# Kernel optimization log

Measured on AMD Instinct MI355X. Metric: run time of the kernel, lower is better.

The kernel has to match this reference:

```python
import math
import jax, jax.numpy as jnp
import numpy as np

B, C_IN, H, W = 16, 384, 64, 64
CDIM, K, NSCALES, ITERS = 128, 64, 2, 3

def conv1x1(x, w, b):
    # x: [B,C,H,W], w: [O,C], b: [O]
    return jnp.einsum('bchw,oc->bohw', x, w) + b[None, :, None, None]

def mlp2(x, w1, b1, w2, b2):
    return conv1x1(jax.nn.relu(conv1x1(x, w1, b1)), w2, b2)

def log_optimal_transport(scores, dustbin, iters):
    B_, K_, N_ = scores.shape
    Z = jnp.concatenate([scores, dustbin], axis=1)  # [B,K+1,N]
    log_mu = jnp.full((B_, K_ + 1), -math.log(K_ + 1), dtype=scores.dtype)
    log_nu = jnp.full((B_, N_), -math.log(N_), dtype=scores.dtype)
    u = jnp.zeros_like(log_mu)
    v = jnp.zeros_like(log_nu)
    for _ in range(iters):
        u = log_mu - jax.nn.logsumexp(Z + v[:, None, :], axis=2)
        v = log_nu - jax.nn.logsumexp(Z + u[:, :, None], axis=1)
    return Z + u[:, :, None] + v[:, None, :]

def avg_pool2(x):
    b, c, h, w = x.shape
    return x.reshape(b, c, h // 2, 2, w // 2, 2).mean(axis=(3, 5))

def scale_branch(xs, fw1, fb1, fw2, fb2, sw1, sb1, sw2, sb2, dw1, db1, dw2, db2):
    b = xs.shape[0]
    local_feat = mlp2(xs, fw1, fb1, fw2, fb2).reshape(b, CDIM, -1)   # [B,C,N]
    score = mlp2(xs, sw1, sb1, sw2, sb2).reshape(b, K, -1)           # [B,K,N]
    dustbin = mlp2(xs, dw1, db1, dw2, db2).reshape(b, 1, -1)         # [B,1,N]
    log_p = log_optimal_transport(score, dustbin, ITERS)
    p = jnp.exp(log_p)[:, :-1, :]                                    # drop dustbin row
    p = p / (p.sum(axis=-1, keepdims=True) + 1e-8)
    out = jnp.einsum('bcn,bkn->bck', local_feat, p)                  # [B,C,K]
    out = out / jnp.clip(jnp.linalg.norm(out, axis=1, keepdims=True), 1e-12)
    return out.reshape(b, -1), local_feat

def setup_inputs():
    key = jax.random.key(0)
    ks = jax.random.split(key, 13)
    inp = {'x': jax.random.normal(ks[0], (B, C_IN, H, W), jnp.float32)}
    kidx = 1
    for s in range(NSCALES):
        for name, (o, i) in [('fw1', (512, C_IN)), ('fw2', (CDIM, 512)),
                              ('sw1', (512, C_IN)), ('sw2', (K, 512)),
                              ('dw1', (128, C_IN)), ('dw2', (1, 128))]:
            inp[f'{name}_{s}'] = 0.02 * jax.random.normal(ks[kidx % 13], (o, i), jnp.float32)
            inp[f'{name[0]}b{name[2]}_{s}'] = jnp.zeros((o,), jnp.float32)
            kidx += 1
    return inp

def reference(x,
              fw1_0, fb1_0, fw2_0, fb2_0, sw1_0, sb1_0, sw2_0, sb2_0, dw1_0, db1_0, dw2_0, db2_0,
              fw1_1, fb1_1, fw2_1, fb2_1, sw1_1, sb1_1, sw2_1, sb2_1, dw1_1, db1_1, dw2_1, db2_1):
    params = [
        (fw1_0, fb1_0, fw2_0, fb2_0, sw1_0, sb1_0, sw2_0, sb2_0, dw1_0, db1_0, dw2_0, db2_0),
        (fw1_1, fb1_1, fw2_1, fb2_1, sw1_1, sb1_1, sw2_1, sb2_1, dw1_1, db1_1, dw2_1, db2_1),
    ]
    descs = []
    xs = x
    for s in range(NSCALES):
        if s > 0:
            xs = avg_pool2(xs)
        d, _ = scale_branch(xs, *params[s])
        descs.append(d)
    g = jnp.stack(descs, axis=1).mean(axis=1)
    g = g / jnp.clip(jnp.linalg.norm(g, axis=1, keepdims=True), 1e-12)
    return g
```

## Files before the change

### kernel.cpp

```cpp
#include <hip/hip_runtime.h>
#include <math.h>

typedef __attribute__((ext_vector_type(8))) short short8;
typedef __attribute__((ext_vector_type(4))) float floatx4;

__device__ inline float bf2f(short s) {
    union { unsigned u; float f; } x; x.u = ((unsigned)(unsigned short)s) << 16; return x.f;
}
__device__ inline short f2bf(float f) {
    union { float f; unsigned u; } x; x.f = f;
    unsigned r = x.u + 0x7fff + ((x.u >> 16) & 1);
    return (short)(r >> 16);
}

struct WSet {
    const float *fw1, *fb1, *fw2, *sw1, *sb1, *sw2, *sb2, *dw1, *db1, *dw2, *db2;
};

__global__ __launch_bounds__(256) void wprep(WSet a0, WSet a1,
    short* __restrict__ W1f, short* __restrict__ W2af, short* __restrict__ W2bf,
    float* __restrict__ B1p, float* __restrict__ B2bp)
{
    const int s = blockIdx.y;
    const WSet A = s ? a1 : a0;
    W1f  += (size_t)s * 491520;
    W2af += (size_t)s * 65536;
    W2bf += (size_t)s * 98304;
    B1p  += s * 1280;
    B2bp += s * 128;
    int id = blockIdx.x * 256 + threadIdx.x;
    if (id < 491520) {
        int e = id & 7, l = (id >> 3) & 63, g = (id >> 9) & 15, rest = id >> 13;
        int kc = rest % 12, c = rest / 12;
        int m = c * 256 + g * 16 + (l & 15);
        int k = kc * 32 + (l >> 4) * 8 + e;
        float v = 0.f;
        if (m < 512) v = A.fw1[m * 384 + k];
        else if (m < 1024) v = A.sw1[(m - 512) * 384 + k];
        else if (m < 1152) v = A.dw1[(m - 1024) * 384 + k];
        W1f[id] = f2bf(v);
        return;
    }
    id -= 491520;
    if (id < 65536) {
        int e = id & 7, l = (id >> 3) & 63, g = (id >> 9) & 7, ka = id >> 12;
        int r = g * 16 + (l & 15), k = ka * 32 + (l >> 4) * 8 + e;
        W2af[id] = f2bf(A.fw2[r * 512 + k]);
        return;
    }
    id -= 65536;
    if (id < 98304) {
        int e = id & 7, l = (id >> 3) & 63, g = (id >> 9) & 7, kb = id >> 12;
        int r = g * 16 + (l & 15), krel = kb * 32 + (l >> 4) * 8 + e;
        float v = 0.f;
        if (r < 64 && krel < 512) v = A.sw2[r * 512 + krel];
        else if (r == 64 && krel >= 512 && krel < 640) v = A.dw2[krel - 512];
        W2bf[id] = f2bf(v);
        return;
    }
    id -= 98304;
    if (id < 1280) {
        float v = 0.f;
        if (id < 512) v = A.fb1[id];
        else if (id < 1024) v = A.sb1[id - 512];
        else if (id < 1152) v = A.db1[id - 1024];
        B1p[id] = v;
        return;
    }
    id -= 1280;
    if (id < 128) B2bp[id] = id < 64 ? A.sb2[id] : id == 64 ? A.db2[0] : 0.f;
}

__global__ __launch_bounds__(256) void xprep(const float* __restrict__ x,
                                             short* __restrict__ xT, short* __restrict__ x1T)
{
    __shared__ float xt[64 * 129];
    const int ip = blockIdx.x;
    const int cg = blockIdx.y;
    const int b  = blockIdx.z;
    const int t  = threadIdx.x;
    #pragma unroll
    for (int u = 0; u < 8; u++) {
        int idx = t + 256 * u;
        int c = idx >> 5, spq = idx & 31;
        float4 v = *(const float4*)&x[(((long)b * 384 + cg * 64 + c) * 64 + ip * 2 + (spq >> 4)) * 64 + (spq & 15) * 4];
        float* d = &xt[c * 129 + spq * 4];
        d[0] = v.x; d[1] = v.y; d[2] = v.z; d[3] = v.w;
    }
    __syncthreads();
    {
        int sp = t >> 1, ch = t & 1;
        short tmp[32];
        #pragma unroll
        for (int cc = 0; cc < 32; cc++) tmp[cc] = f2bf(xt[(ch * 32 + cc) * 129 + sp]);
        short* dst = xT + ((long)b * 4096 + ip * 128 + sp) * 384 + cg * 64 + ch * 32;
        #pragma unroll
        for (int v = 0; v < 4; v++) *(short8*)(dst + v * 8) = *(short8*)(tmp + v * 8);
    }
    {
        int j1 = t >> 3, c8 = t & 7;
        short tmp[8];
        #pragma unroll
        for (int e = 0; e < 8; e++) {
            int c = c8 * 8 + e;
            float v = 0.25f * (xt[c * 129 + j1 * 2]      + xt[c * 129 + j1 * 2 + 1] +
                               xt[c * 129 + 64 + j1 * 2] + xt[c * 129 + 64 + j1 * 2 + 1]);
            tmp[e] = f2bf(v);
        }
        *(short8*)(x1T + ((long)b * 1024 + ip * 32 + j1) * 384 + cg * 64 + c8 * 8) = *(short8*)tmp;
    }
}

__global__ __launch_bounds__(512, 4) void fused_mlp(
    const short* __restrict__ W1f_, const float* __restrict__ B1p_,
    const short* __restrict__ W2af_, const float* __restrict__ fb2_0, const float* __restrict__ fb2_1,
    const short* __restrict__ W2bf_, const float* __restrict__ B2bp_,
    const short* __restrict__ xT, const short* __restrict__ x1T,
    float* __restrict__ feat0, float* __restrict__ feat1,
    short* __restrict__ Eg0, short* __restrict__ Eg1,
    float* __restrict__ pu0, float* __restrict__ pu1)
{
    __shared__ short xs[12 * 2048];
    __shared__ short hs[8 * 2048];
    const int tid = threadIdx.x;
    const int wid = tid >> 6, lane = tid & 63;
    const int l15 = lane & 15, q = lane >> 4;
    const int bx = blockIdx.x, b = blockIdx.y;
    const int sc = bx >= 64;
    const int tile = sc ? bx - 64 : bx;
    const int N = sc ? 1024 : 4096;
    const int n0 = tile * 64;
    const short* XT = sc ? x1T : xT;
    const short* W1f = W1f_ + (size_t)sc * 491520;
    const float* B1p = B1p_ + sc * 1280;
    const short* W2af = W2af_ + (size_t)sc * 65536;
    const short* W2bf = W2bf_ + (size_t)sc * 98304;
    const float* fb2 = sc ? fb2_1 : fb2_0;
    const float* B2bp = B2bp_ + sc * 128;
    float* feat = (sc ? feat1 : feat0) + (long)b * 128 * N;
    short* Eg = (sc ? Eg1 : Eg0) + (long)b * 65 * N;
    float* pu = sc ? pu1 : pu0;
    const int npart = sc ? 16 : 64;

    {
        const int n = tid >> 3;
        const int c0 = (tid & 7) * 6;
        const short* src = XT + ((long)b * N + n0 + n) * 384 + c0 * 8;
        const int jj = n >> 4, nl = n & 15;
        #pragma unroll
        for (int i = 0; i < 6; i++) {
            int c = c0 + i;
            int kc = c >> 2, qq = c & 3;
            *(short8*)(xs + kc * 2048 + jj * 512 + ((qq << 4) | nl) * 8) =
                *(const short8*)(src + i * 8);
        }
    }
    __syncthreads();

    floatx4 acc2[2][4];
    #pragma unroll
    for (int i = 0; i < 2; i++)
        #pragma unroll
        for (int j = 0; j < 4; j++) acc2[i][j] = floatx4{0.f, 0.f, 0.f, 0.f};

    auto phase2 = [&](int pc) {
        if (pc < 2) {
            const short* WA = W2af + (size_t)pc * 32768;
            short8 hb[2][4], wa[2];
            #pragma unroll
            for (int j = 0; j < 4; j++) hb[0][j] = *(short8*)(hs + j * 512 + lane * 8);
            wa[0] = *(const short8*)(WA + wid * 512 + lane * 8);
            #pragma unroll
            for (int kc2 = 0; kc2 < 8; kc2++) {
                short8 bfr[4];
                #pragma unroll
                for (int j = 0; j < 4; j++) bfr[j] = hb[kc2 & 1][j];
                short8 aF = wa[kc2 & 1];
                if (kc2 + 1 < 8) {
                    #pragma unroll
                    for (int j = 0; j < 4; j++)
                        hb[(kc2 + 1) & 1][j] = *(short8*)(hs + (kc2 + 1) * 2048 + j * 512 + lane * 8);
                    wa[(kc2 + 1) & 1] = *(const short8*)(WA + ((kc2 + 1) * 8 + wid) * 512 + lane * 8);
                }
                #pragma unroll
                for (int j = 0; j < 4; j++)
                    acc2[0][j] = __builtin_amdgcn_mfma_f32_16x16x32_bf16(aF, bfr[j], acc2[0][j], 0, 0, 0);
            }
        } else {
            if (wid >= 5) return;
            const short* WB = W2bf + (size_t)(pc - 2) * 32768;
            short8 hb[2][4], we[2];
            #pragma unroll
            for (int j = 0; j < 4; j++) hb[0][j] = *(short8*)(hs + j * 512 + lane * 8);
            we[0] = *(const short8*)(WB + wid * 512 + lane * 8);
            #pragma unroll
            for (int kc2 = 0; kc2 < 8; kc2++) {
                short8 bfr[4];
                #pragma unroll
                for (int j = 0; j < 4; j++) bfr[j] = hb[kc2 & 1][j];
                short8 aE = we[kc2 & 1];
                if (kc2 + 1 < 8) {
                    #pragma unroll
                    for (int j = 0; j < 4; j++)
                        hb[(kc2 + 1) & 1][j] = *(short8*)(hs + (kc2 + 1) * 2048 + j * 512 + lane * 8);
                    we[(kc2 + 1) & 1] = *(const short8*)(WB + ((kc2 + 1) * 8 + wid) * 512 + lane * 8);
                }
                #pragma unroll
                for (int j = 0; j < 4; j++)
                    acc2[1][j] = __builtin_amdgcn_mfma_f32_16x16x32_bf16(aE, bfr[j], acc2[1][j], 0, 0, 0);
            }
        }
    };

    for (int c = 0; c < 5; c++) {
        if (c > 0) phase2(c - 1);
        floatx4 acc1[2][4];
        #pragma unroll
        for (int i = 0; i < 2; i++)
            #pragma unroll
            for (int j = 0; j < 4; j++) acc1[i][j] = floatx4{0.f, 0.f, 0.f, 0.f};
        const short* Wb = W1f + (long)c * 98304;
        short8 abuf[2][2];
        #pragma unroll
        for (int i = 0; i < 2; i++) {
            abuf[0][i] = *(const short8*)(Wb + (wid * 2 + i) * 512 + lane * 8);
            abuf[1][i] = *(const short8*)(Wb + (16 + wid * 2 + i) * 512 + lane * 8);
        }
        #pragma unroll
        for (int kc = 0; kc < 12; kc++) {
            short8 ac[2], bc[4];
            #pragma unroll
            for (int i = 0; i < 2; i++) ac[i] = abuf[kc & 1][i];
            #pragma unroll
            for (int j = 0; j < 4; j++) bc[j] = *(short8*)(xs + kc * 2048 + j * 512 + lane * 8);
            if (kc + 2 < 12) {
                #pragma unroll
                for (int i = 0; i < 2; i++)
                    abuf[kc & 1][i] = *(const short8*)(Wb + ((kc + 2) * 16 + wid * 2 + i) * 512 + lane * 8);
            }
            #pragma unroll
            for (int i = 0; i < 2; i++)
                #pragma unroll
                for (int j = 0; j < 4; j++)
                    acc1[i][j] = __builtin_amdgcn_mfma_f32_16x16x32_bf16(ac[i], bc[j], acc1[i][j], 0, 0, 0);
        }
        __syncthreads();
        #pragma unroll
        for (int i = 0; i < 2; i++) {
            const int qf = i * 2 + (q >> 1);
            const int e0 = 4 * (q & 1);
            const int mrow = c * 256 + wid * 32 + i * 16 + q * 4;
            float bw[4];
            #pragma unroll
            for (int rr = 0; rr < 4; rr++) bw[rr] = B1p[mrow + rr];
            #pragma unroll
            for (int j = 0; j < 4; j++) {
                short pk[4];
                #pragma unroll
                for (int rr = 0; rr < 4; rr++)
                    pk[rr] = f2bf(fmaxf(acc1[i][j][rr] + bw[rr], 0.f));
                *(unsigned long long*)(hs + wid * 2048 + j * 512 + ((qf << 4) | l15) * 8 + e0) =
                    *(unsigned long long*)pk;
            }
        }
        __syncthreads();
    }
    phase2(4);

    {
        const int row0 = wid * 16 + q * 4;
        #pragma unroll
        for (int rr = 0; rr < 4; rr++) {
            float bv = fb2[row0 + rr];
            #pragma unroll
            for (int j = 0; j < 4; j++)
                feat[(long)(row0 + rr) * N + n0 + 16 * j + l15] = acc2[0][j][rr] + bv;
        }
    }
    __syncthreads();
    float* puld = (float*)hs;
    if (wid < 4) {
        #pragma unroll
        for (int rr = 0; rr < 4; rr++) {
            int row = wid * 16 + q * 4 + rr;
            float bv = B2bp[row];
            float s = 0.f;
            #pragma unroll
            for (int j = 0; j < 4; j++) {
                float e = expf(acc2[1][j][rr] + bv);
                Eg[(long)row * N + n0 + 16 * j + l15] = f2bf(e);
                s += e;
            }
            s += __shfl_xor(s, 1); s += __shfl_xor(s, 2);
            s += __shfl_xor(s, 4); s += __shfl_xor(s, 8);
            if (l15 == 0) puld[row] = s;
        }
    } else if (wid == 4) {
        #pragma unroll
        for (int rr = 0; rr < 4; rr++) {
            int row = 64 + q * 4 + rr;
            bool valid = (row == 64);
            float bv = B2bp[64];
            float s = 0.f;
            #pragma unroll
            for (int j = 0; j < 4; j++) {
                float e = expf(acc2[1][j][rr] + bv);
                if (valid) {
                    Eg[(long)64 * N + n0 + 16 * j + l15] = f2bf(e);
                    s += e;
                }
            }
            s += __shfl_xor(s, 1); s += __shfl_xor(s, 2);
            s += __shfl_xor(s, 4); s += __shfl_xor(s, 8);
            if (valid && l15 == 0) puld[64] = s;
        }
    }
    __syncthreads();
    if (tid < 65)
        pu[((long)b * npart + tile) * 65 + tid] = puld[tid];
}

__global__ __launch_bounds__(256) void sk_step(
    const short* __restrict__ Eg0, const short* __restrict__ Eg1,
    const float* __restrict__ pin0, const float* __restrict__ pin1,
    float* __restrict__ pout0, float* __restrict__ pout1, int nin0, int nin1)
{
    __shared__ short Es[65 * 264];
    __shared__ float evs[256];
    __shared__ float eus[65];
    const int t = threadIdx.x;
    const int bx = blockIdx.x, b = blockIdx.y;
    const int sc = bx >= 16;
    const int chunk = sc ? bx - 16 : bx;
    const int N = sc ? 1024 : 4096;
    const float invN = sc ? (1.0f / 1024.0f) : (1.0f / 4096.0f);
    const int n0 = chunk * 256;
    const short* Eb = (sc ? Eg1 : Eg0) + (long)b * 65 * N;
    const float* pin = sc ? pin1 : pin0;
    const int nin = sc ? nin1 : nin0;
    float* pout = sc ? pout1 : pout0;
    const int nout = sc ? 4 : 16;
    if (t < 65) {
        float s = 0.f;
        for (int ch = 0; ch < nin; ch++) s += pin[((long)b * nin + ch) * 65 + t];
        eus[t] = (1.0f / 65.0f) / s;
    }
    for (int it = t; it < 2080; it += 256) {
        int k = it >> 5, n8 = it & 31;
        *(short8*)(Es + k * 264 + n8 * 8) = *(const short8*)(Eb + (long)k * N + n0 + n8 * 8);
    }
    __syncthreads();
    float sv = 0.f;
    #pragma unroll 4
    for (int k = 0; k < 65; k++) sv += bf2f(Es[k * 264 + t]) * eus[k];
    evs[t] = invN / sv;
    __syncthreads();
    const int wid = t >> 6, lane = t & 63;
    for (int k = wid; k < 65; k += 4) {
        const short* er = Es + k * 264 + lane * 4;
        float4 v4 = *(const float4*)&evs[lane * 4];
        float s = bf2f(er[0]) * v4.x + bf2f(er[1]) * v4.y + bf2f(er[2]) * v4.z + bf2f(er[3]) * v4.w;
        #pragma unroll
        for (int off = 32; off >= 1; off >>= 1) s += __shfl_xor(s, off);
        if (lane == 0) pout[((long)b * nout + chunk) * 65 + k] = s;
    }
}

__global__ __launch_bounds__(256) void sk_desc(
    const short* __restrict__ Eg0, const short* __restrict__ Eg1,
    const float* __restrict__ pin0, const float* __restrict__ pin1,
    const float* __restrict__ feat0, const float* __restrict__ feat1,
    float* __restrict__ part0, float* __restrict__ part1, int nin0, int nin1)
{
    __shared__ short Es[65 * 264];
    __shared__ float eus[65];
    const int t = threadIdx.x;
    const int bx = blockIdx.x, b = blockIdx.y;
    const int sc = bx >= 16;
    const int chunk = sc ? bx - 16 : bx;
    const int N = sc ? 1024 : 4096;
    const float invN = sc ? (1.0f / 1024.0f) : (1.0f / 4096.0f);
    const int nch = sc ? 4 : 16;
    const int n0 = chunk * 256;
    const short* Eb = (sc ? Eg1 : Eg0) + (long)b * 65 * N;
    const float* pin = sc ? pin1 : pin0;
    const int nin = sc ? nin1 : nin0;
    const float* fb = (sc ? feat1 : feat0) + (long)b * 128 * N;
    float* part = sc ? part1 : part0;
    if (t < 65) {
        float s = 0.f;
        for (int ch = 0; ch < nin; ch++) s += pin[((long)b * nin + ch) * 65 + t];
        eus[t] = (1.0f / 65.0f) / s;
    }
    for (int it = t; it < 2080; it += 256) {
        int k = it >> 5, n8 = it & 31;
        *(short8*)(Es + k * 264 + n8 * 8) = *(const short8*)(Eb + (long)k * N + n0 + n8 * 8);
    }
    __syncthreads();
    float sv = 0.f;
    #pragma unroll 4
    for (int k = 0; k < 65; k++) sv += bf2f(Es[k * 264 + t]) * eus[k];
    float evt = invN / sv;
    #pragma unroll 4
    for (int k = 0; k < 64; k++)
        Es[k * 264 + t] = f2bf(bf2f(Es[k * 264 + t]) * eus[k] * evt);
    __syncthreads();
    const int wid = t >> 6, lane = t & 63;
    const int l15 = lane & 15, q = lane >> 4;
    float* pb = part + ((long)b * nch + chunk) * 8256;
    for (int k = wid; k < 64; k += 4) {
        const short* er = Es + k * 264 + lane * 4;
        float s = bf2f(er[0]) + bf2f(er[1]) + bf2f(er[2]) + bf2f(er[3]);
        #pragma unroll
        for (int off = 32; off >= 1; off >>= 1) s += __shfl_xor(s, off);
        if (lane == 0) pb[8192 + k] = s;
    }
    floatx4 acc[2][4];
    #pragma unroll
    for (int mt = 0; mt < 2; mt++)
        #pragma unroll
        for (int nt = 0; nt < 4; nt++) acc[mt][nt] = floatx4{0.f, 0.f, 0.f, 0.f};
    #pragma unroll 2
    for (int ks = 0; ks < 8; ks++) {
        short8 ah[2], al[2];
        #pragma unroll
        for (int mt = 0; mt < 2; mt++) {
            const float* fp = fb + (long)(wid * 32 + mt * 16 + l15) * N + n0 + ks * 32 + q * 8;
            float4 v0 = *(const float4*)fp;
            float4 v1 = *(const float4*)(fp + 4);
            float va[8] = {v0.x, v0.y, v0.z, v0.w, v1.x, v1.y, v1.z, v1.w};
            short hh[8], ll[8];
            #pragma unroll
            for (int e = 0; e < 8; e++) {
                short h = f2bf(va[e]);
                hh[e] = h;
                ll[e] = f2bf(va[e] - bf2f(h));
            }
            ah[mt] = *(short8*)hh;
            al[mt] = *(short8*)ll;
        }
        #pragma unroll
        for (int nt = 0; nt < 4; nt++) {
            short8 bfr = *(short8*)(Es + (nt * 16 + l15) * 264 + ks * 32 + q * 8);
            #pragma unroll
            for (int mt = 0; mt < 2; mt++) {
                acc[mt][nt] = __builtin_amdgcn_mfma_f32_16x16x32_bf16(al[mt], bfr, acc[mt][nt], 0, 0, 0);
                acc[mt][nt] = __builtin_amdgcn_mfma_f32_16x16x32_bf16(ah[mt], bfr, acc[mt][nt], 0, 0, 0);
            }
        }
    }
    #pragma unroll
    for (int mt = 0; mt < 2; mt++)
        #pragma unroll
        for (int nt = 0; nt < 4; nt++)
            #pragma unroll
            for (int rr = 0; rr < 4; rr++)
                pb[(wid * 32 + mt * 16 + q * 4 + rr) * 64 + nt * 16 + l15] = acc[mt][nt][rr];
}

__global__ __launch_bounds__(256) void desc_reduce(
    const float* __restrict__ part0, const float* __restrict__ part1,
    float* __restrict__ desc0, float* __restrict__ desc1, int b0)
{
    __shared__ float cred[4][8];
    const int bx = blockIdx.x, b = blockIdx.y;
    const int sc = bx >= 4;
    const int kg = (bx & 3) * 16;
    const int nch = sc ? 4 : 16;
    const float* pb = (sc ? part1 : part0) + (long)b * nch * 8256;
    float* desc = sc ? desc1 : desc0;
    const int t = threadIdx.x;
    const int c = t & 127, kh = t >> 7;
    float a[8], rs[8];
    #pragma unroll
    for (int j = 0; j < 8; j++) { a[j] = 0.f; rs[j] = 0.f; }
    for (int ch = 0; ch < nch; ch++) {
        const float* p = pb + (long)ch * 8256;
        #pragma unroll
        for (int j = 0; j < 8; j++) a[j] += p[c * 64 + kg + kh * 8 + j];
        #pragma unroll
        for (int j = 0; j < 8; j++) rs[j] += p[8192 + kg + kh * 8 + j];
    }
    float sq[8];
    #pragma unroll
    for (int j = 0; j < 8; j++) {
        a[j] *= 1.0f / (rs[j] + 1e-8f);
        sq[j] = a[j] * a[j];
    }
    #pragma unroll
    for (int off = 32; off >= 1; off >>= 1)
        #pragma unroll
        for (int j = 0; j < 8; j++) sq[j] += __shfl_xor(sq[j], off);
    if ((t & 63) == 0) {
        #pragma unroll
        for (int j = 0; j < 8; j++) cred[t >> 6][j] = sq[j];
    }
    __syncthreads();
    float* d = desc + (long)(b0 + b) * 8192;
    #pragma unroll
    for (int j = 0; j < 8; j++) {
        float tot = cred[kh * 2][j] + cred[kh * 2 + 1][j];
        float inv = 1.0f / fmaxf(sqrtf(tot), 1e-12f);
        d[c * 64 + kg + kh * 8 + j] = a[j] * inv;
    }
}

__global__ __launch_bounds__(256) void final_kernel(const float* __restrict__ desc0,
                                                    const float* __restrict__ desc1,
                                                    float* __restrict__ out)
{
    __shared__ float red[4];
    const int b = blockIdx.x;
    const float* d0 = desc0 + (long)b * 8192;
    const float* d1 = desc1 + (long)b * 8192;
    float s = 0;
    for (int i = threadIdx.x; i < 8192; i += 256) {
        float t = (d0[i] + d1[i]) * 0.5f; s += t * t;
    }
    const int wave = threadIdx.x >> 6, lane = threadIdx.x & 63;
    #pragma unroll
    for (int off = 32; off >= 1; off >>= 1) s += __shfl_xor(s, off);
    if (lane == 0) red[wave] = s;
    __syncthreads();
    float tot = red[0] + red[1] + red[2] + red[3];
    float inv = 1.0f / fmaxf(sqrtf(tot), 1e-12f);
    for (int i = threadIdx.x; i < 8192; i += 256)
        out[(long)b * 8192 + i] = (d0[i] + d1[i]) * 0.5f * inv;
}

extern "C" void kernel_launch(void* const* d_in, const int* in_sizes, int n_in,
                              void* d_out, int out_size, void* d_ws, size_t ws_size,
                              hipStream_t stream)
{
    (void)in_sizes; (void)n_in; (void)out_size;
    const float* x = (const float*)d_in[0];
    WSet ws2[2];
    const float* fb2p[2];
    for (int s = 0; s < 2; s++) {
        int o = 1 + s * 12;
        ws2[s].fw1 = (const float*)d_in[o + 0];  ws2[s].fb1 = (const float*)d_in[o + 1];
        ws2[s].fw2 = (const float*)d_in[o + 2];  fb2p[s]    = (const float*)d_in[o + 3];
        ws2[s].sw1 = (const float*)d_in[o + 4];  ws2[s].sb1 = (const float*)d_in[o + 5];
        ws2[s].sw2 = (const float*)d_in[o + 6];  ws2[s].sb2 = (const float*)d_in[o + 7];
        ws2[s].dw1 = (const float*)d_in[o + 8];  ws2[s].db1 = (const float*)d_in[o + 9];
        ws2[s].dw2 = (const float*)d_in[o + 10]; ws2[s].db2 = (const float*)d_in[o + 11];
    }

    const size_t fixed = ((size_t)2*491520*2 + 2*65536*2 + 2*98304*2
                        + 2*1280*4 + 2*128*4 + (size_t)2*16*8192*4) + (1 << 16);
    const size_t perb = (size_t)4096*384*2 + (size_t)1024*384*2
                      + (size_t)128*4096*4 + (size_t)128*1024*4
                      + (size_t)65*4096*2 + (size_t)65*1024*2
                      + (size_t)(64+16)*65*4 + (size_t)(16+4)*65*4
                      + (size_t)16*8256*4 + (size_t)4*8256*4 + 8192;
    int CB = 4;
    const int cand[3] = {16, 8, 4};
    for (int ci = 0; ci < 3; ci++)
        if (fixed + (size_t)cand[ci] * perb <= ws_size) { CB = cand[ci]; break; }

    char* p = (char*)d_ws;
    auto alloc = [&](size_t bytes) -> char* {
        char* r = p; p += (bytes + 255) & ~(size_t)255; return r;
    };
    short* W1f   = (short*)alloc((size_t)2 * 491520 * 2);
    short* W2af  = (short*)alloc((size_t)2 * 65536 * 2);
    short* W2bf  = (short*)alloc((size_t)2 * 98304 * 2);
    float* B1p   = (float*)alloc((size_t)2 * 1280 * 4);
    float* B2bp  = (float*)alloc((size_t)2 * 128 * 4);
    float* desc0 = (float*)alloc((size_t)16 * 8192 * 4);
    float* desc1 = (float*)alloc((size_t)16 * 8192 * 4);
    short* xT    = (short*)alloc((size_t)CB * 4096 * 384 * 2);
    short* x1T   = (short*)alloc((size_t)CB * 1024 * 384 * 2);
    float* feat0 = (float*)alloc((size_t)CB * 128 * 4096 * 4);
    float* feat1 = (float*)alloc((size_t)CB * 128 * 1024 * 4);
    short* Eg0   = (short*)alloc((size_t)CB * 65 * 4096 * 2);
    short* Eg1   = (short*)alloc((size_t)CB * 65 * 1024 * 2);
    float* puA0  = (float*)alloc((size_t)CB * 64 * 65 * 4);
    float* puA1  = (float*)alloc((size_t)CB * 16 * 65 * 4);
    float* puB0  = (float*)alloc((size_t)CB * 16 * 65 * 4);
    float* puB1  = (float*)alloc((size_t)CB * 4 * 65 * 4);
    float* part0 = (float*)alloc((size_t)CB * 16 * 8256 * 4);
    float* part1 = (float*)alloc((size_t)CB * 4 * 8256 * 4);

    wprep<<<dim3(2566, 2), 256, 0, stream>>>(ws2[0], ws2[1], W1f, W2af, W2bf, B1p, B2bp);

    for (int b0 = 0; b0 < 16; b0 += CB) {
        xprep<<<dim3(32, 6, CB), 256, 0, stream>>>(x + (size_t)b0 * 384 * 4096, xT, x1T);
        fused_mlp<<<dim3(80, CB), 512, 0, stream>>>(
            W1f, B1p, W2af, fb2p[0], fb2p[1], W2bf, B2bp,
            xT, x1T, feat0, feat1, Eg0, Eg1, puA0, puA1);
        sk_step<<<dim3(20, CB), 256, 0, stream>>>(Eg0, Eg1, puA0, puA1, puB0, puB1, 64, 16);
        sk_step<<<dim3(20, CB), 256, 0, stream>>>(Eg0, Eg1, puB0, puB1, puA0, puA1, 16, 4);
        sk_desc<<<dim3(20, CB), 256, 0, stream>>>(Eg0, Eg1, puA0, puA1,
                                                  feat0, feat1, part0, part1, 16, 4);
        desc_reduce<<<dim3(8, CB), 256, 0, stream>>>(part0, part1, desc0, desc1, b0);
    }
    final_kernel<<<16, 256, 0, stream>>>(desc0, desc1, (float*)d_out);
}
```

Measured before the change: 395.1 us.

## Merge prep kernels, fuse Sinkhorn steps, retile MLP phase1, fold scaling into desc

Weight and input prep are merged into a single launch, and the two Sinkhorn step kernels are replaced by one sk2x kernel with a block per scale and batch that iterates in place. The first-layer MLP warp tiling changes to a 4x2 layout across M and N, so each warp loads fewer shared-memory B fragments. sk_desc now applies the u and v scalings through vectors instead of rewriting E in shared memory. sk2x uses only 32 blocks, so the serialized Sinkhorn work may underuse the GPU.

```diff
diff --git a/kernel.cpp b/kernel.cpp
--- a/kernel.cpp
+++ b/kernel.cpp
@@ -17,18 +17,10 @@
     const float *fw1, *fb1, *fw2, *sw1, *sb1, *sw2, *sb2, *dw1, *db1, *dw2, *db2;
 };
 
-__global__ __launch_bounds__(256) void wprep(WSet a0, WSet a1,
+__device__ inline void wprep_core(const WSet A,
     short* __restrict__ W1f, short* __restrict__ W2af, short* __restrict__ W2bf,
-    float* __restrict__ B1p, float* __restrict__ B2bp)
-{
-    const int s = blockIdx.y;
-    const WSet A = s ? a1 : a0;
-    W1f  += (size_t)s * 491520;
-    W2af += (size_t)s * 65536;
-    W2bf += (size_t)s * 98304;
-    B1p  += s * 1280;
-    B2bp += s * 128;
-    int id = blockIdx.x * 256 + threadIdx.x;
+    float* __restrict__ B1p, float* __restrict__ B2bp, int id)
+{
     if (id < 491520) {
         int e = id & 7, l = (id >> 3) & 63, g = (id >> 9) & 15, rest = id >> 13;
         int kc = rest % 12, c = rest / 12;
@@ -71,14 +63,10 @@
     if (id < 128) B2bp[id] = id < 64 ? A.sb2[id] : id == 64 ? A.db2[0] : 0.f;
 }
 
-__global__ __launch_bounds__(256) void xprep(const float* __restrict__ x,
-                                             short* __restrict__ xT, short* __restrict__ x1T)
-{
-    __shared__ float xt[64 * 129];
-    const int ip = blockIdx.x;
-    const int cg = blockIdx.y;
-    const int b  = blockIdx.z;
-    const int t  = threadIdx.x;
+__device__ inline void xprep_core(const float* __restrict__ x,
+                                  short* __restrict__ xT, short* __restrict__ x1T,
+                                  float* xt, int ip, int cg, int b, int t)
+{
     #pragma unroll
     for (int u = 0; u < 8; u++) {
         int idx = t + 256 * u;
@@ -108,6 +96,43 @@
             tmp[e] = f2bf(v);
         }
         *(short8*)(x1T + ((long)b * 1024 + ip * 32 + j1) * 384 + cg * 64 + c8 * 8) = *(short8*)tmp;
+    }
+}
+
+__global__ __launch_bounds__(256) void wprep(WSet a0, WSet a1,
+    short* __restrict__ W1f, short* __restrict__ W2af, short* __restrict__ W2bf,
+    float* __restrict__ B1p, float* __restrict__ B2bp)
+{
+    const int s = blockIdx.y;
+    const WSet A = s ? a1 : a0;
+    wprep_core(A, W1f + (size_t)s * 491520, W2af + (size_t)s * 65536,
+               W2bf + (size_t)s * 98304, B1p + s * 1280, B2bp + s * 128,
+               blockIdx.x * 256 + threadIdx.x);
+}
+
+__global__ __launch_bounds__(256) void xprep(const float* __restrict__ x,
+                                             short* __restrict__ xT, short* __restrict__ x1T)
+{
+    __shared__ float xt[64 * 129];
+    xprep_core(x, xT, x1T, xt, blockIdx.x, blockIdx.y, blockIdx.z, threadIdx.x);
+}
+
+__global__ __launch_bounds__(256) void prep(WSet a0, WSet a1,
+    short* __restrict__ W1f, short* __restrict__ W2af, short* __restrict__ W2bf,
+    float* __restrict__ B1p, float* __restrict__ B2bp,
+    const float* __restrict__ x, short* __restrict__ xT, short* __restrict__ x1T)
+{
+    __shared__ float xt[64 * 129];
+    const int bid = blockIdx.x, t = threadIdx.x;
+    if (bid < 5132) {
+        const int s = bid >= 2566;
+        const WSet A = s ? a1 : a0;
+        wprep_core(A, W1f + (size_t)s * 491520, W2af + (size_t)s * 65536,
+                   W2bf + (size_t)s * 98304, B1p + s * 1280, B2bp + s * 128,
+                   (bid - (s ? 2566 : 0)) * 256 + t);
+    } else {
+        const int xb = bid - 5132;
+        xprep_core(x, xT, x1T, xt, xb & 31, (xb >> 5) % 6, (xb >> 5) / 6, t);
     }
 }
 
@@ -125,6 +150,7 @@
     const int tid = threadIdx.x;
     const int wid = tid >> 6, lane = tid & 63;
     const int l15 = lane & 15, q = lane >> 4;
+    const int mg = wid >> 1, ng = wid & 1;
     const int bx = blockIdx.x, b = blockIdx.y;
     const int sc = bx >= 64;
     const int tile = sc ? bx - 64 : bx;
@@ -214,52 +240,55 @@
 
     for (int c = 0; c < 5; c++) {
         if (c > 0) phase2(c - 1);
-        floatx4 acc1[2][4];
-        #pragma unroll
-        for (int i = 0; i < 2; i++)
-            #pragma unroll
-            for (int j = 0; j < 4; j++) acc1[i][j] = floatx4{0.f, 0.f, 0.f, 0.f};
+        floatx4 acc1[4][2];
+        #pragma unroll
+        for (int i = 0; i < 4; i++)
+            #pragma unroll
+            for (int j = 0; j < 2; j++) acc1[i][j] = floatx4{0.f, 0.f, 0.f, 0.f};
         const short* Wb = W1f + (long)c * 98304;
-        short8 abuf[2][2];
-        #pragma unroll
-        for (int i = 0; i < 2; i++) {
-            abuf[0][i] = *(const short8*)(Wb + (wid * 2 + i) * 512 + lane * 8);
-            abuf[1][i] = *(const short8*)(Wb + (16 + wid * 2 + i) * 512 + lane * 8);
+        short8 abuf[2][4];
+        #pragma unroll
+        for (int i = 0; i < 4; i++) {
+            abuf[0][i] = *(const short8*)(Wb + (mg * 4 + i) * 512 + lane * 8);
+            abuf[1][i] = *(const short8*)(Wb + (16 + mg * 4 + i) * 512 + lane * 8);
         }
         #pragma unroll
         for (int kc = 0; kc < 12; kc++) {
-            short8 ac[2], bc[4];
-            #pragma unroll
-            for (int i = 0; i < 2; i++) ac[i] = abuf[kc & 1][i];
-            #pragma unroll
-            for (int j = 0; j < 4; j++) bc[j] = *(short8*)(xs + kc * 2048 + j * 512 + lane * 8);
+            short8 ac[4], bc[2];
+            #pragma unroll
+            for (int i = 0; i < 4; i++) ac[i] = abuf[kc & 1][i];
+            #pragma unroll
+            for (int j = 0; j < 2; j++)
+                bc[j] = *(short8*)(xs + kc * 2048 + (ng * 2 + j) * 512 + lane * 8);
             if (kc + 2 < 12) {
                 #pragma unroll
-                for (int i = 0; i < 2; i++)
-                    abuf[kc & 1][i] = *(const short8*)(Wb + ((kc + 2) * 16 + wid * 2 + i) * 512 + lane * 8);
-            }
-            #pragma unroll
-            for (int i = 0; i < 2; i++)
+                for (int i = 0; i < 4; i++)
+                    abuf[kc & 1][i] = *(const short8*)(Wb + ((kc + 2) * 16 + mg * 4 + i) * 512 + lane * 8);
+            }
+            #pragma unroll
+            for (int i = 0; i < 4; i++)
                 #pragma unroll
-                for (int j = 0; j < 4; j++)
+                for (int j = 0; j < 2; j++)
                     acc1[i][j] = __builtin_amdgcn_mfma_f32_16x16x32_bf16(ac[i], bc[j], acc1[i][j], 0, 0, 0);
         }
         __syncthreads();
         #pragma unroll
-        for (int i = 0; i < 2; i++) {
-            const int qf = i * 2 + (q >> 1);
+        for (int i = 0; i < 4; i++) {
+            const int kc2 = mg * 2 + (i >> 1);
+            const int qf = (i & 1) * 2 + (q >> 1);
             const int e0 = 4 * (q & 1);
-            const int mrow = c * 256 + wid * 32 + i * 16 + q * 4;
+            const int mrow = c * 256 + mg * 64 + i * 16 + q * 4;
             float bw[4];
             #pragma unroll
             for (int rr = 0; rr < 4; rr++) bw[rr] = B1p[mrow + rr];
             #pragma unroll
-            for (int j = 0; j < 4; j++) {
+            for (int j = 0; j < 2; j++) {
+                const int jj = ng * 2 + j;
                 short pk[4];
                 #pragma unroll
                 for (int rr = 0; rr < 4; rr++)
                     pk[rr] = f2bf(fmaxf(acc1[i][j][rr] + bw[rr], 0.f));
-                *(unsigned long long*)(hs + wid * 2048 + j * 512 + ((qf << 4) | l15) * 8 + e0) =
+                *(unsigned long long*)(hs + kc2 * 2048 + jj * 512 + ((qf << 4) | l15) * 8 + e0) =
                     *(unsigned long long*)pk;
             }
         }
@@ -320,49 +349,55 @@
         pu[((long)b * npart + tile) * 65 + tid] = puld[tid];
 }
 
-__global__ __launch_bounds__(256) void sk_step(
+__global__ __launch_bounds__(512) void sk2x(
     const short* __restrict__ Eg0, const short* __restrict__ Eg1,
-    const float* __restrict__ pin0, const float* __restrict__ pin1,
-    float* __restrict__ pout0, float* __restrict__ pout1, int nin0, int nin1)
-{
-    __shared__ short Es[65 * 264];
-    __shared__ float evs[256];
-    __shared__ float eus[65];
+    const float* __restrict__ puA0, const float* __restrict__ puA1,
+    float* __restrict__ pu3_0, float* __restrict__ pu3_1)
+{
+    __shared__ float ev[4096];
+    __shared__ float eus[72];
     const int t = threadIdx.x;
-    const int bx = blockIdx.x, b = blockIdx.y;
-    const int sc = bx >= 16;
-    const int chunk = sc ? bx - 16 : bx;
+    const int sc = blockIdx.x, b = blockIdx.y;
     const int N = sc ? 1024 : 4096;
     const float invN = sc ? (1.0f / 1024.0f) : (1.0f / 4096.0f);
-    const int n0 = chunk * 256;
     const short* Eb = (sc ? Eg1 : Eg0) + (long)b * 65 * N;
-    const float* pin = sc ? pin1 : pin0;
-    const int nin = sc ? nin1 : nin0;
-    float* pout = sc ? pout1 : pout0;
-    const int nout = sc ? 4 : 16;
+    const float* pin = sc ? puA1 : puA0;
+    const int nin = sc ? 16 : 64;
+    float* pout = sc ? pu3_1 : pu3_0;
     if (t < 65) {
         float s = 0.f;
         for (int ch = 0; ch < nin; ch++) s += pin[((long)b * nin + ch) * 65 + t];
         eus[t] = (1.0f / 65.0f) / s;
     }
-    for (int it = t; it < 2080; it += 256) {
-        int k = it >> 5, n8 = it & 31;
-        *(short8*)(Es + k * 264 + n8 * 8) = *(const short8*)(Eb + (long)k * N + n0 + n8 * 8);
-    }
-    __syncthreads();
-    float sv = 0.f;
-    #pragma unroll 4
-    for (int k = 0; k < 65; k++) sv += bf2f(Es[k * 264 + t]) * eus[k];
-    evs[t] = invN / sv;
     __syncthreads();
     const int wid = t >> 6, lane = t & 63;
-    for (int k = wid; k < 65; k += 4) {
-        const short* er = Es + k * 264 + lane * 4;
-        float4 v4 = *(const float4*)&evs[lane * 4];
-        float s = bf2f(er[0]) * v4.x + bf2f(er[1]) * v4.y + bf2f(er[2]) * v4.z + bf2f(er[3]) * v4.w;
-        #pragma unroll
-        for (int off = 32; off >= 1; off >>= 1) s += __shfl_xor(s, off);
-        if (lane == 0) pout[((long)b * nout + chunk) * 65 + k] = s;
+    #pragma unroll
+    for (int it = 0; it < 2; it++) {
+        for (int n4 = t; n4 * 4 < N; n4 += 512) {
+            const int n = n4 * 4;
+            float s0 = 0.f, s1 = 0.f, s2 = 0.f, s3 = 0.f;
+            for (int k = 0; k < 65; k++) {
+                short4 e4 = *(const short4*)(Eb + (long)k * N + n);
+                float eu = eus[k];
+                s0 += bf2f(e4.x) * eu; s1 += bf2f(e4.y) * eu;
+                s2 += bf2f(e4.z) * eu; s3 += bf2f(e4.w) * eu;
+            }
+            ev[n] = invN / s0; ev[n + 1] = invN / s1;
+            ev[n + 2] = invN / s2; ev[n + 3] = invN / s3;
+        }
+        __syncthreads();
+        for (int k = wid; k < 65; k += 8) {
+            const short* er = Eb + (long)k * N;
+            float s = 0.f;
+            for (int n = lane; n < N; n += 64) s += bf2f(er[n]) * ev[n];
+            #pragma unroll
+            for (int off = 32; off >= 1; off >>= 1) s += __shfl_xor(s, off);
+            if (lane == 0) {
+                if (it == 0) eus[k] = (1.0f / 65.0f) / s;
+                else pout[(long)b * 65 + k] = s;
+            }
+        }
+        __syncthreads();
     }
 }
 
@@ -374,6 +409,7 @@
 {
     __shared__ short Es[65 * 264];
     __shared__ float eus[65];
+    __shared__ float evs[256];
     const int t = threadIdx.x;
     const int bx = blockIdx.x, b = blockIdx.y;
     const int sc = bx >= 16;
@@ -400,20 +436,18 @@
     float sv = 0.f;
     #pragma unroll 4
     for (int k = 0; k < 65; k++) sv += bf2f(Es[k * 264 + t]) * eus[k];
-    float evt = invN / sv;
-    #pragma unroll 4
-    for (int k = 0; k < 64; k++)
-        Es[k * 264 + t] = f2bf(bf2f(Es[k * 264 + t]) * eus[k] * evt);
+    evs[t] = invN / sv;
     __syncthreads();
     const int wid = t >> 6, lane = t & 63;
     const int l15 = lane & 15, q = lane >> 4;
     float* pb = part + ((long)b * nch + chunk) * 8256;
     for (int k = wid; k < 64; k += 4) {
         const short* er = Es + k * 264 + lane * 4;
-        float s = bf2f(er[0]) + bf2f(er[1]) + bf2f(er[2]) + bf2f(er[3]);
+        float4 v4 = *(const float4*)&evs[lane * 4];
+        float s = bf2f(er[0]) * v4.x + bf2f(er[1]) * v4.y + bf2f(er[2]) * v4.z + bf2f(er[3]) * v4.w;
         #pragma unroll
         for (int off = 32; off >= 1; off >>= 1) s += __shfl_xor(s, off);
-        if (lane == 0) pb[8192 + k] = s;
+        if (lane == 0) pb[8192 + k] = s * eus[k];
     }
     floatx4 acc[2][4];
     #pragma unroll
@@ -422,6 +456,9 @@
         for (int nt = 0; nt < 4; nt++) acc[mt][nt] = floatx4{0.f, 0.f, 0.f, 0.f};
     #pragma unroll 2
     for (int ks = 0; ks < 8; ks++) {
+        float4 ev0 = *(const float4*)&evs[ks * 32 + q * 8];
+        float4 ev1 = *(const float4*)&evs[ks * 32 + q * 8 + 4];
+        float evq[8] = {ev0.x, ev0.y, ev0.z, ev0.w, ev1.x, ev1.y, ev1.z, ev1.w};
         short8 ah[2], al[2];
         #pragma unroll
         for (int mt = 0; mt < 2; mt++) {
@@ -432,9 +469,10 @@
             short hh[8], ll[8];
             #pragma unroll
             for (int e = 0; e < 8; e++) {
-                short h = f2bf(va[e]);
+                float sv2 = va[e] * evq[e];
+                short h = f2bf(sv2);
                 hh[e] = h;
-                ll[e] = f2bf(va[e] - bf2f(h));
+                ll[e] = f2bf(sv2 - bf2f(h));
             }
             ah[mt] = *(short8*)hh;
             al[mt] = *(short8*)ll;
@@ -450,12 +488,14 @@
         }
     }
     #pragma unroll
-    for (int mt = 0; mt < 2; mt++)
-        #pragma unroll
-        for (int nt = 0; nt < 4; nt++)
+    for (int nt = 0; nt < 4; nt++) {
+        float euk = eus[nt * 16 + l15];
+        #pragma unroll
+        for (int mt = 0; mt < 2; mt++)
             #pragma unroll
             for (int rr = 0; rr < 4; rr++)
-                pb[(wid * 32 + mt * 16 + q * 4 + rr) * 64 + nt * 16 + l15] = acc[mt][nt][rr];
+                pb[(wid * 32 + mt * 16 + q * 4 + rr) * 64 + nt * 16 + l15] = acc[mt][nt][rr] * euk;
+    }
 }
 
 __global__ __launch_bounds__(256) void desc_reduce(
@@ -582,18 +622,29 @@
     float* part0 = (float*)alloc((size_t)CB * 16 * 8256 * 4);
     float* part1 = (float*)alloc((size_t)CB * 4 * 8256 * 4);
 
-    wprep<<<dim3(2566, 2), 256, 0, stream>>>(ws2[0], ws2[1], W1f, W2af, W2bf, B1p, B2bp);
-
-    for (int b0 = 0; b0 < 16; b0 += CB) {
-        xprep<<<dim3(32, 6, CB), 256, 0, stream>>>(x + (size_t)b0 * 384 * 4096, xT, x1T);
-        fused_mlp<<<dim3(80, CB), 512, 0, stream>>>(
+    if (CB == 16) {
+        prep<<<dim3(8204), 256, 0, stream>>>(ws2[0], ws2[1],
+            W1f, W2af, W2bf, B1p, B2bp, x, xT, x1T);
+        fused_mlp<<<dim3(80, 16), 512, 0, stream>>>(
             W1f, B1p, W2af, fb2p[0], fb2p[1], W2bf, B2bp,
             xT, x1T, feat0, feat1, Eg0, Eg1, puA0, puA1);
-        sk_step<<<dim3(20, CB), 256, 0, stream>>>(Eg0, Eg1, puA0, puA1, puB0, puB1, 64, 16);
-        sk_step<<<dim3(20, CB), 256, 0, stream>>>(Eg0, Eg1, puB0, puB1, puA0, puA1, 16, 4);
-        sk_desc<<<dim3(20, CB), 256, 0, stream>>>(Eg0, Eg1, puA0, puA1,
-                                                  feat0, feat1, part0, part1, 16, 4);
-        desc_reduce<<<dim3(8, CB), 256, 0, stream>>>(part0, part1, desc0, desc1, b0);
-    }
-    final_kernel<<<16, 256, 0, stream>>>(desc0, desc1, (float*)d_out);
-}
+        sk2x<<<dim3(2, 16), 512, 0, stream>>>(Eg0, Eg1, puA0, puA1, puB0, puB1);
+        sk_desc<<<dim3(20, 16), 256, 0, stream>>>(Eg0, Eg1, puB0, puB1,
+                                                  feat0, feat1, part0, part1, 1, 1);
+        desc_reduce<<<dim3(8, 16), 256, 0, stream>>>(part0, part1, desc0, desc1, 0);
+        final_kernel<<<16, 256, 0, stream>>>(desc0, desc1, (float*)d_out);
+    } else {
+        wprep<<<dim3(2566, 2), 256, 0, stream>>>(ws2[0], ws2[1], W1f, W2af, W2bf, B1p, B2bp);
+        for (int b0 = 0; b0 < 16; b0 += CB) {
+            xprep<<<dim3(32, 6, CB), 256, 0, stream>>>(x + (size_t)b0 * 384 * 4096, xT, x1T);
+            fused_mlp<<<dim3(80, CB), 512, 0, stream>>>(
+                W1f, B1p, W2af, fb2p[0], fb2p[1], W2bf, B2bp,
+                xT, x1T, feat0, feat1, Eg0, Eg1, puA0, puA1);
+            sk2x<<<dim3(2, CB), 512, 0, stream>>>(Eg0, Eg1, puA0, puA1, puB0, puB1);
+            sk_desc<<<dim3(20, CB), 256, 0, stream>>>(Eg0, Eg1, puB0, puB1,
+                                                      feat0, feat1, part0, part1, 1, 1);
+            desc_reduce<<<dim3(8, CB), 256, 0, stream>>>(part0, part1, desc0, desc1, b0);
+        }
+        final_kernel<<<16, 256, 0, stream>>>(desc0, desc1, (float*)d_out);
+    }
+}
```

New measurement: 597.3 us. 51.2% more time.
